# Performance work log

Hardware: AMD Instinct MI355X
Metric: run time of the kernel (lower is better)

The kernel has to match this reference:

```python
import jax, jax.numpy as jnp
import numpy as np

INPUT_SIZE = (128, 384)
DOWNSAMPLE = 4.0


def make_voxels():
    # grid_conf: xbound=[-51.2,51.2,0.4], ybound same, zbound=[-5,3,1]
    dx = jnp.array([0.4, 0.4, 1.0], jnp.float32)
    bx = jnp.array([-51.2 + 0.2, -51.2 + 0.2, -5.0 + 0.5], jnp.float32)
    nx = (256, 256, 8)
    xs = jnp.linspace(bx[0] - dx[0] / 2, bx[0] - dx[0] / 2 + dx[0] * (nx[0] - 1), nx[0], dtype=jnp.float32)
    ys = jnp.linspace(bx[1] - dx[1] / 2, bx[1] - dx[1] / 2 + dx[1] * (nx[1] - 1), nx[1], dtype=jnp.float32)
    zs = jnp.linspace(bx[2] - dx[2] / 2, bx[2] - dx[2] / 2 + dx[2] * (nx[2] - 1), nx[2], dtype=jnp.float32)
    X = jnp.broadcast_to(xs[None, None, :], (nx[2], nx[1], nx[0]))
    Y = jnp.broadcast_to(ys[None, :, None], (nx[2], nx[1], nx[0]))
    Z = jnp.broadcast_to(zs[:, None, None], (nx[2], nx[1], nx[0]))
    return jnp.stack((X, Y, Z), -1)  # [Z, Y, X, 3]


def setup_inputs() -> dict:
    key = jax.random.key(0)
    ks = jax.random.split(key, 8)
    B, N = 4, 6
    eye = jnp.eye(3, dtype=jnp.float32)
    rots = eye + 0.1 * jax.random.normal(ks[0], (B, N, 3, 3), jnp.float32)
    trans = jax.random.normal(ks[1], (B, N, 3), jnp.float32)
    # realistic fisheye intrinsics: fx,fy ~ 300, cx ~ 192, cy ~ 64
    fx = 300.0 + 10.0 * jax.random.normal(ks[2], (B, N), jnp.float32)
    fy = 300.0 + 10.0 * jax.random.normal(ks[3], (B, N), jnp.float32)
    cx = 192.0 + 2.0 * jax.random.normal(ks[4], (B, N), jnp.float32)
    cy = 64.0 + 2.0 * jax.random.normal(ks[5], (B, N), jnp.float32)
    z = jnp.zeros((B, N), jnp.float32)
    o = jnp.ones((B, N), jnp.float32)
    intrins = jnp.stack([
        jnp.stack([fx, z, cx], -1),
        jnp.stack([z, fy, cy], -1),
        jnp.stack([z, z, o], -1),
    ], -2)  # [B,N,3,3]
    distorts = 0.1 * jax.random.uniform(ks[6], (B, N, 8), jnp.float32)
    post_rots = (1.0 / DOWNSAMPLE) * eye + 0.001 * jax.random.normal(ks[7], (B, N, 3, 3), jnp.float32)
    post_trans = 0.1 * jax.random.normal(jax.random.fold_in(key, 99), (B, N, 3), jnp.float32)
    return {
        "voxels": make_voxels(),
        "rots": rots,
        "trans": trans,
        "intrins": intrins,
        "distorts": distorts,
        "post_rots": post_rots,
        "post_trans": post_trans,
    }


def reference(voxels, rots, trans, intrins, distorts, post_rots, post_trans):
    B, N = rots.shape[:2]
    Z, Y, X, _ = voxels.shape
    P = Z * Y * X
    pts = voxels.reshape(1, 1, P, 3)  # broadcast over B,N
    # rotate into camera frame, translate
    pts = jnp.einsum("bnij,uvpj->bnpi", rots, pts) + trans[:, :, None, :]
    # mask points behind camera: x,y -> 9999 (z untouched)
    neg = pts[..., 2:3] < 0
    xy = jnp.where(neg, jnp.float32(9999.0), pts[..., :2])
    depth = pts[..., 2:3]
    xy = xy / depth  # pinhole divide
    # fisheye distortion (k1,k2,k3,k4 at indices 0,1,4,5; p1,p2,k5,k6 unused)
    r = jnp.sqrt(jnp.sum(xy * xy, axis=-1))  # [B,N,P]
    k1 = distorts[..., 0:1]
    k2 = distorts[..., 1:2]
    k3 = distorts[..., 4:5]
    k4 = distorts[..., 5:6]
    t = jnp.arctan2(r, jnp.ones_like(r))
    t2 = t * t
    radial = t * (1 + k1 * t2 + k2 * t2 ** 2 + k3 * t2 ** 3 + k4 * t2 ** 4) / (r + 1e-6)
    xy = xy * radial[..., None]
    pts3 = jnp.concatenate([xy, jnp.ones_like(depth)], axis=-1)
    pts3 = jnp.einsum("bnij,bnpj->bnpi", intrins, pts3)
    # image-space augmentation
    pts3 = jnp.einsum("bnij,bnpj->bnpi", post_rots, pts3) + post_trans[:, :, None, :]
    # [B,N,Z,Y,X,3] -> [B,N,Z,X,Y,3] -> take xy
    pts2 = pts3.reshape(B, N, Z, Y, X, 3).transpose(0, 1, 2, 4, 3, 5)[..., :2]
    # normalize to [-1,1]; feature shape [H/d, W/d] flipped to [W', H']
    feat_hw = jnp.array([INPUT_SIZE[0] / DOWNSAMPLE, INPUT_SIZE[1] / DOWNSAMPLE], jnp.float32)
    wh = jnp.flip(feat_hw)
    pts2 = pts2 / (wh - 1) * 2 - 1
    return pts2.reshape(B * N * Z, X, Y, 2)
```

## Files before the change

kernel.cpp:

```cpp
#include <hip/hip_runtime.h>
#include <math.h>

#define ZD 8
#define YD 256
#define XD 256

__global__ __launch_bounds__(256) void splat_kernel(
    const float* __restrict__ voxels,
    const float* __restrict__ rots,
    const float* __restrict__ trans,
    const float* __restrict__ intrins,
    const float* __restrict__ distorts,
    const float* __restrict__ post_rots,
    const float* __restrict__ post_trans,
    float* __restrict__ out)
{
    const int y  = threadIdx.x;
    const int L  = blockIdx.x;
    const int x  = L & 255;
    const int z  = (L >> 8) & 7;
    const int bn = L >> 11;

    const float vx = voxels[3 * x];
    const float vy = voxels[768 * y + 1];
    const float vz = voxels[196608 * z + 2];

    const float* R  = rots       + bn * 9;
    const float* T  = trans      + bn * 3;
    const float* I  = intrins    + bn * 9;
    const float* D  = distorts   + bn * 8;
    const float* PR = post_rots  + bn * 9;
    const float* PT = post_trans + bn * 3;

    const float p0 = R[0]*vx + R[1]*vy + R[2]*vz + T[0];
    const float p1 = R[3]*vx + R[4]*vy + R[5]*vz + T[1];
    const float p2 = R[6]*vx + R[7]*vy + R[8]*vz + T[2];

    const bool neg = (p2 < 0.0f);
    float xy0 = neg ? 9999.0f : p0;
    float xy1 = neg ? 9999.0f : p1;
    xy0 = xy0 / p2;
    xy1 = xy1 / p2;

    const float r  = sqrtf(xy0*xy0 + xy1*xy1);
    const float k1 = D[0], k2 = D[1], k3 = D[4], k4 = D[5];
    const float t  = atanf(r);
    const float t2 = t * t;
    const float t4 = t2 * t2;
    const float t6 = t4 * t2;
    const float t8 = t4 * t4;
    const float radial = t * (1.0f + k1*t2 + k2*t4 + k3*t6 + k4*t8) / (r + 1e-6f);
    xy0 *= radial;
    xy1 *= radial;

    const float i0 = I[0]*xy0 + I[1]*xy1 + I[2];
    const float i1 = I[3]*xy0 + I[4]*xy1 + I[5];
    const float i2 = I[6]*xy0 + I[7]*xy1 + I[8];

    const float q0 = PR[0]*i0 + PR[1]*i1 + PR[2]*i2 + PT[0];
    const float q1 = PR[3]*i0 + PR[4]*i1 + PR[5]*i2 + PT[1];

    const float o0 = q0 / 95.0f * 2.0f - 1.0f;
    const float o1 = q1 / 31.0f * 2.0f - 1.0f;

    const size_t off = ((size_t)((bn * 8 + z) * 256 + x)) * 256 + y;
    reinterpret_cast<float2*>(out)[off] = make_float2(o0, o1);
}

extern "C" void kernel_launch(void* const* d_in, const int* in_sizes, int n_in,
                              void* d_out, int out_size, void* d_ws, size_t ws_size,
                              hipStream_t stream) {
    const float* voxels     = (const float*)d_in[0];
    const float* rots       = (const float*)d_in[1];
    const float* trans      = (const float*)d_in[2];
    const float* intrins    = (const float*)d_in[3];
    const float* distorts   = (const float*)d_in[4];
    const float* post_rots  = (const float*)d_in[5];
    const float* post_trans = (const float*)d_in[6];
    float* out = (float*)d_out;

    const int nblocks = 24 * ZD * XD;
    splat_kernel<<<dim3(nblocks), dim3(256), 0, stream>>>(
        voxels, rots, trans, intrins, distorts, post_rots, post_trans, out);
}
```

Before: 146.2 us.

## Process two points per thread with fast atan/rcp approximations and float4 stores

```diff
diff --git a/kernel.cpp b/kernel.cpp
--- a/kernel.cpp
+++ b/kernel.cpp
@@ -1,11 +1,26 @@
 #include <hip/hip_runtime.h>
 #include <math.h>
 
+
 #define ZD 8
-#define YD 256
-#define XD 256
 
-__global__ __launch_bounds__(256) void splat_kernel(
+__device__ __forceinline__ float fast_rcp(float x) {
+    return __builtin_amdgcn_rcpf(x);
+}
+
+__device__ __forceinline__ float fast_atan_pos(float r) {
+    const bool big = r > 1.0f;
+    const float u  = big ? fast_rcp(r) : r;
+    const float u2 = u * u;
+    float p = fmaf(u2, 0.0208351f, -0.0851330f);
+    p = fmaf(u2, p, 0.1801410f);
+    p = fmaf(u2, p, -0.3302995f);
+    p = fmaf(u2, p, 0.9998660f);
+    const float a = u * p;
+    return big ? (1.57079632679489662f - a) : a;
+}
+
+__global__ __launch_bounds__(128) void splat_kernel(
     const float* __restrict__ voxels,
     const float* __restrict__ rots,
     const float* __restrict__ trans,
@@ -15,15 +30,17 @@
     const float* __restrict__ post_trans,
     float* __restrict__ out)
 {
-    const int y  = threadIdx.x;
+    const int t  = threadIdx.x;
     const int L  = blockIdx.x;
     const int x  = L & 255;
     const int z  = (L >> 8) & 7;
     const int bn = L >> 11;
 
-    const float vx = voxels[3 * x];
-    const float vy = voxels[768 * y + 1];
-    const float vz = voxels[196608 * z + 2];
+    const float vx  = voxels[3 * x];
+    const float vz  = voxels[196608 * z + 2];
+    const int   y0  = 2 * t;
+    const float vy0 = voxels[768 * y0 + 1];
+    const float vy1 = voxels[768 * y0 + 768 + 1];
 
     const float* R  = rots       + bn * 9;
     const float* T  = trans      + bn * 3;
@@ -32,39 +49,51 @@
     const float* PR = post_rots  + bn * 9;
     const float* PT = post_trans + bn * 3;
 
-    const float p0 = R[0]*vx + R[1]*vy + R[2]*vz + T[0];
-    const float p1 = R[3]*vx + R[4]*vy + R[5]*vz + T[1];
-    const float p2 = R[6]*vx + R[7]*vy + R[8]*vz + T[2];
+    const float b0 = fmaf(R[0], vx, fmaf(R[2], vz, T[0]));
+    const float b1 = fmaf(R[3], vx, fmaf(R[5], vz, T[1]));
+    const float b2 = fmaf(R[6], vx, fmaf(R[8], vz, T[2]));
 
-    const bool neg = (p2 < 0.0f);
-    float xy0 = neg ? 9999.0f : p0;
-    float xy1 = neg ? 9999.0f : p1;
-    xy0 = xy0 / p2;
-    xy1 = xy1 / p2;
+    const float k1 = D[0], k2 = D[1], k3 = D[4], k4 = D[5];
 
-    const float r  = sqrtf(xy0*xy0 + xy1*xy1);
-    const float k1 = D[0], k2 = D[1], k3 = D[4], k4 = D[5];
-    const float t  = atanf(r);
-    const float t2 = t * t;
-    const float t4 = t2 * t2;
-    const float t6 = t4 * t2;
-    const float t8 = t4 * t4;
-    const float radial = t * (1.0f + k1*t2 + k2*t4 + k3*t6 + k4*t8) / (r + 1e-6f);
-    xy0 *= radial;
-    xy1 *= radial;
+    float res[4];
 
-    const float i0 = I[0]*xy0 + I[1]*xy1 + I[2];
-    const float i1 = I[3]*xy0 + I[4]*xy1 + I[5];
-    const float i2 = I[6]*xy0 + I[7]*xy1 + I[8];
+#pragma unroll
+    for (int j = 0; j < 2; ++j) {
+        const float vy = (j == 0) ? vy0 : vy1;
+        const float p0 = fmaf(R[1], vy, b0);
+        const float p1 = fmaf(R[4], vy, b1);
+        const float p2 = fmaf(R[7], vy, b2);
 
-    const float q0 = PR[0]*i0 + PR[1]*i1 + PR[2]*i2 + PT[0];
-    const float q1 = PR[3]*i0 + PR[4]*i1 + PR[5]*i2 + PT[1];
+        const bool  neg  = (p2 < 0.0f);
+        const float rcpz = fast_rcp(p2);
+        float xy0 = (neg ? 9999.0f : p0) * rcpz;
+        float xy1 = (neg ? 9999.0f : p1) * rcpz;
 
-    const float o0 = q0 / 95.0f * 2.0f - 1.0f;
-    const float o1 = q1 / 31.0f * 2.0f - 1.0f;
+        const float r  = __builtin_amdgcn_sqrtf(fmaf(xy0, xy0, xy1 * xy1));
+        const float th = fast_atan_pos(r);
+        const float t2 = th * th;
+        float poly = fmaf(t2, k4, k3);
+        poly = fmaf(t2, poly, k2);
+        poly = fmaf(t2, poly, k1);
+        poly = fmaf(t2, poly, 1.0f);
+        const float radial = th * poly * fast_rcp(r + 1e-6f);
+        xy0 *= radial;
+        xy1 *= radial;
 
-    const size_t off = ((size_t)((bn * 8 + z) * 256 + x)) * 256 + y;
-    reinterpret_cast<float2*>(out)[off] = make_float2(o0, o1);
+        const float i0 = fmaf(I[0], xy0, fmaf(I[1], xy1, I[2]));
+        const float i1 = fmaf(I[3], xy0, fmaf(I[4], xy1, I[5]));
+        const float i2 = fmaf(I[6], xy0, fmaf(I[7], xy1, I[8]));
+
+        const float q0 = fmaf(PR[0], i0, fmaf(PR[1], i1, fmaf(PR[2], i2, PT[0])));
+        const float q1 = fmaf(PR[3], i0, fmaf(PR[4], i1, fmaf(PR[5], i2, PT[1])));
+
+        res[2 * j]     = fmaf(q0, 2.0f / 95.0f, -1.0f);
+        res[2 * j + 1] = fmaf(q1, 2.0f / 31.0f, -1.0f);
+    }
+
+    const size_t off4 = ((size_t)((bn * ZD + z) * 256 + x)) * 128 + t;
+    reinterpret_cast<float4*>(out)[off4] =
+        make_float4(res[0], res[1], res[2], res[3]);
 }
 
 extern "C" void kernel_launch(void* const* d_in, const int* in_sizes, int n_in,
@@ -79,7 +108,7 @@
     const float* post_trans = (const float*)d_in[6];
     float* out = (float*)d_out;
 
-    const int nblocks = 24 * ZD * XD;
-    splat_kernel<<<dim3(nblocks), dim3(256), 0, stream>>>(
+    const int nblocks = 24 * ZD * 256;
+    splat_kernel<<<dim3(nblocks), dim3(128), 0, stream>>>(
         voxels, rots, trans, intrins, distorts, post_rots, post_trans, out);
 }
```

New measurement: 132.8 us. -9.2%, faster.
